# Kernel tuning notes

Measured on AMD Instinct MI355X. Metric: run time of the kernel, lower is better.

The kernel has to match this reference:

```python
import jax, jax.numpy as jnp
import numpy as np

N = 8192        # nodes
E = 131072      # random edges (16 * N); self loops appended inside reference
D = 128         # in_channels
K = int(np.ceil(0.5 * N))  # pooled nodes, ratio=0.5
NEG = 0.2       # leaky relu negative slope


def setup_inputs() -> dict:
    key = jax.random.key(0)
    ks = jax.random.split(key, 10)
    s = 0.05
    return dict(
        x=jax.random.normal(ks[0], (N, D), jnp.float32),
        edge_src=jax.random.randint(ks[1], (E,), 0, N),
        edge_off=jax.random.randint(ks[2], (E,), 0, N - 1),
        W_lin=jax.random.normal(ks[3], (D, D), jnp.float32) * s,
        b_lin=jnp.zeros((D,), jnp.float32),
        w_att=jax.random.normal(ks[4], (2 * D,), jnp.float32) * s,
        b_att=jnp.zeros((1,), jnp.float32),
        w1=jax.random.normal(ks[5], (D,), jnp.float32) * s,
        b1=jnp.zeros((1,), jnp.float32),
        w2=jax.random.normal(ks[6], (D,), jnp.float32) * s,
        w3=jax.random.normal(ks[7], (D,), jnp.float32) * s,
        b3=jnp.zeros((1,), jnp.float32),
    )


def reference(x, edge_src, edge_off, W_lin, b_lin, w_att, b_att, w1, b1, w2, w3, b3):
    # build edges with guaranteed no self loops, then add_remaining_self_loops (weight 1)
    dst = (edge_src + 1 + edge_off) % N
    loop = jnp.arange(N)
    row = jnp.concatenate([edge_src, loop])   # [Et] source j
    col = jnp.concatenate([dst, loop])        # [Et] target i
    ew = jnp.ones(row.shape, x.dtype)         # edge weights (fill_value=1)

    # GNN=None -> x_pool = x
    x_pool_j = x[row]                                             # [Et, D]
    x_q = jax.ops.segment_max(x_pool_j, col, num_segments=N)      # scatter-max at target
    x_q = (x_q @ W_lin + b_lin)[col]                              # [Et, D]

    score = jnp.concatenate([x_q, x_pool_j], axis=-1) @ w_att + b_att[0]  # [Et]
    score = jax.nn.leaky_relu(score, negative_slope=NEG)
    # edge softmax over incoming edges of each target node (stable)
    smax = jax.ops.segment_max(score, col, num_segments=N)
    e = jnp.exp(score - smax[col])
    score = e / jax.ops.segment_sum(e, col, num_segments=N)[col]
    # dropout p=0 (eval): no-op

    # attention-weighted aggregation
    x_new = jax.ops.segment_sum(x[row] * score[:, None], col, num_segments=N)  # [N, D]

    # LEConv fitness (out_channels=1): lin3(x) + sum_j w_ji * (lin1(x)_i - lin2(x)_j)
    a = x_new @ w1 + b1[0]                                        # [N]
    b = x_new @ w2                                                # [N]
    agg = jax.ops.segment_sum(ew * (a[col] - b[row]), col, num_segments=N)
    fitness = jax.nn.sigmoid(x_new @ w3 + b3[0] + agg)            # [N]

    # topk pooling (single graph): k = ceil(ratio * N)
    perm = jnp.argsort(-fitness)[:K]
    x_out = x_new[perm] * fitness[perm][:, None]                  # [K, D]

    # dense N x N attention as in original, then column-select perm
    attention = jnp.zeros((N, N), x.dtype).at[row, col].set(score)
    S_perm = attention[:, perm]                                   # [N, K] == S[:, perm]

    # A_new = S^T A S (A sparse, weight 1 per edge incl. self loops), diag removed
    T = jax.ops.segment_sum(ew[:, None] * S_perm[col], row, num_segments=N)  # A @ S_perm
    A_new = S_perm.T @ T                                          # [K, K]
    A_new = A_new * (1.0 - jnp.eye(K, dtype=x.dtype))             # remove_diag

    return x_out, A_new, perm, S_perm
```

## Files before the change

### kernel.cpp

```cpp
#include <hip/hip_runtime.h>
#include <hip/hip_bf16.h>
#include <math.h>
#include <stdint.h>

#define N_NODES 8192
#define E_EDGES 131072
#define D_DIM 128
#define M_EDGES (E_EDGES + N_NODES)
#define K_TOP 4096
#define NEG_SLOPE 0.2

__global__ __launch_bounds__(256) void k_zero(uint4* __restrict__ p, int n16) {
    int i = blockIdx.x * 256 + threadIdx.x;
    if (i < n16) { uint4 z; z.x = 0u; z.y = 0u; z.z = 0u; z.w = 0u; p[i] = z; }
}

__global__ void k_init_edges(const int* __restrict__ edge_src, const int* __restrict__ edge_off,
                             unsigned* __restrict__ rowA, unsigned* __restrict__ colA,
                             unsigned* __restrict__ dup,
                             unsigned* __restrict__ col_cnt, unsigned* __restrict__ row_cnt) {
    int e = blockIdx.x * blockDim.x + threadIdx.x;
    if (e >= M_EDGES) return;
    unsigned r, c;
    if (e < E_EDGES) {
        r = (unsigned)edge_src[e];
        c = (r + 1u + (unsigned)edge_off[e]) % N_NODES;
    } else {
        r = c = (unsigned)(e - E_EDGES);
    }
    rowA[e] = r; colA[e] = c; dup[e] = 0u;
    atomicAdd(&col_cnt[c], 1u);
    atomicAdd(&row_cnt[r], 1u);
}

__global__ __launch_bounds__(1024) void k_scan2(const unsigned* __restrict__ cnt0, unsigned* __restrict__ off0, unsigned* __restrict__ cur0,
                                                const unsigned* __restrict__ cnt1, unsigned* __restrict__ off1, unsigned* __restrict__ cur1) {
    const unsigned* cnt = blockIdx.x ? cnt1 : cnt0;
    unsigned* off = blockIdx.x ? off1 : off0;
    unsigned* cur = blockIdx.x ? cur1 : cur0;
    __shared__ unsigned part[1024];
    const int n = N_NODES, per = N_NODES / 1024;
    int t = threadIdx.x;
    unsigned local[8];
    unsigned s = 0;
    for (int j = 0; j < per; j++) { local[j] = cnt[t * per + j]; s += local[j]; }
    part[t] = s; __syncthreads();
    for (int d = 1; d < 1024; d <<= 1) {
        unsigned v = (t >= d) ? part[t - d] : 0u;
        __syncthreads();
        part[t] += v;
        __syncthreads();
    }
    unsigned run = (t > 0) ? part[t - 1] : 0u;
    for (int j = 0; j < per; j++) {
        off[t * per + j] = run;
        if (cur) cur[t * per + j] = run;
        run += local[j];
    }
    if (t == 1023) off[n] = run;
}

__global__ void k_fill(const unsigned* __restrict__ rowA, const unsigned* __restrict__ colA,
                       unsigned* __restrict__ col_cur, unsigned* __restrict__ row_cur,
                       unsigned* __restrict__ col_edges, unsigned* __restrict__ row_edges) {
    int e = blockIdx.x * blockDim.x + threadIdx.x;
    if (e >= M_EDGES) return;
    unsigned p1 = atomicAdd(&col_cur[colA[e]], 1u); col_edges[p1] = (unsigned)e;
    unsigned p2 = atomicAdd(&row_cur[rowA[e]], 1u); row_edges[p2] = (unsigned)e;
}

__global__ __launch_bounds__(128) void k_lin(const float* __restrict__ x,
                                             const unsigned* __restrict__ col_off,
                                             const unsigned* __restrict__ col_edges,
                                             const unsigned* __restrict__ rowA,
                                             unsigned* __restrict__ dup,
                                             const float* __restrict__ W, const float* __restrict__ b_lin,
                                             const float* __restrict__ w_att,
                                             double* __restrict__ q_score, double* __restrict__ k_score) {
    int c = blockIdx.x, t = threadIdx.x;
    __shared__ unsigned rloc[256];
    __shared__ float xq[128];
    __shared__ double red[4];
    int lo = (int)col_off[c], hi = (int)col_off[c + 1];
    int n = hi - lo;
    for (int i = t; i < n && i < 256; i += 128) rloc[i] = rowA[col_edges[lo + i]];
    __syncthreads();
    for (int i = t; i < n; i += 128) {
        unsigned ri = (i < 256) ? rloc[i] : rowA[col_edges[lo + i]];
        for (int j = 0; j < i; j++) {
            unsigned rj = (j < 256) ? rloc[j] : rowA[col_edges[lo + j]];
            if (rj == ri) { dup[col_edges[lo + i]] = 1u; break; }
        }
    }
    float m = -INFINITY;
    for (int i = 0; i < n; i++) {
        unsigned r = (i < 256) ? rloc[i] : rowA[col_edges[lo + i]];
        m = fmaxf(m, x[(size_t)r * D_DIM + t]);
    }
    xq[t] = m;
    __syncthreads();
    double acc = (double)b_lin[t];
    for (int j = 0; j < D_DIM; j++) acc += (double)xq[j] * (double)W[j * D_DIM + t];
    double q = acc * (double)w_att[t];
    double k = (double)x[(size_t)c * D_DIM + t] * (double)w_att[D_DIM + t];
    for (int o = 32; o > 0; o >>= 1) { q += __shfl_down(q, o); k += __shfl_down(k, o); }
    if ((t & 63) == 0) { red[t >> 6] = q; red[2 + (t >> 6)] = k; }
    __syncthreads();
    if (t == 0) { q_score[c] = red[0] + red[1]; k_score[c] = red[2] + red[3]; }
}

__global__ __launch_bounds__(128) void k_sm_xnew(const float* __restrict__ x,
                                                 const unsigned* __restrict__ col_off,
                                                 const unsigned* __restrict__ col_edges,
                                                 const unsigned* __restrict__ rowA,
                                                 const double* __restrict__ q_score,
                                                 const double* __restrict__ k_score,
                                                 const float* __restrict__ b_att,
                                                 const float* __restrict__ w1, const float* __restrict__ b1,
                                                 const float* __restrict__ w2, const float* __restrict__ w3,
                                                 const float* __restrict__ b3,
                                                 double* __restrict__ score_d, float* __restrict__ score_f,
                                                 float* __restrict__ x_new, double* __restrict__ aV,
                                                 double* __restrict__ bV, double* __restrict__ finV) {
    int c = blockIdx.x, t = threadIdx.x;
    __shared__ unsigned eloc[256];
    __shared__ unsigned rloc[256];
    __shared__ double sloc[256];
    __shared__ double redd[2];
    __shared__ double red6[6];
    int lo = (int)col_off[c], hi = (int)col_off[c + 1];
    int n = hi - lo;
    for (int i = t; i < n && i < 256; i += 128) {
        unsigned e = col_edges[lo + i];
        eloc[i] = e;
        rloc[i] = rowA[e];
    }
    __syncthreads();
    double qc = q_score[c] + (double)b_att[0];
    double m = -INFINITY;
    for (int i = t; i < n; i += 128) {
        unsigned r = (i < 256) ? rloc[i] : rowA[col_edges[lo + i]];
        double s = qc + k_score[r];
        s = (s >= 0.0) ? s : NEG_SLOPE * s;
        m = fmax(m, s);
    }
    for (int o = 32; o > 0; o >>= 1) m = fmax(m, __shfl_xor(m, o));
    if ((t & 63) == 0) redd[t >> 6] = m;
    __syncthreads();
    m = fmax(redd[0], redd[1]);
    __syncthreads();
    double sum = 0.0;
    for (int i = t; i < n; i += 128) {
        unsigned r = (i < 256) ? rloc[i] : rowA[col_edges[lo + i]];
        double s = qc + k_score[r];
        s = (s >= 0.0) ? s : NEG_SLOPE * s;
        sum += exp(s - m);
    }
    for (int o = 32; o > 0; o >>= 1) sum += __shfl_xor(sum, o);
    if ((t & 63) == 0) redd[t >> 6] = sum;
    __syncthreads();
    sum = redd[0] + redd[1];
    for (int i = t; i < n; i += 128) {
        unsigned e = (i < 256) ? eloc[i] : col_edges[lo + i];
        unsigned r = (i < 256) ? rloc[i] : rowA[e];
        double s = qc + k_score[r];
        s = (s >= 0.0) ? s : NEG_SLOPE * s;
        double w = exp(s - m) / sum;
        if (i < 256) sloc[i] = w;
        score_d[e] = w;
        score_f[e] = (float)w;
    }
    __syncthreads();
    int d = t;
    double acc = 0.0;
    for (int i = 0; i < n; i++) {
        unsigned r;
        double sc;
        if (i < 256) { r = rloc[i]; sc = sloc[i]; }
        else { unsigned e = col_edges[lo + i]; r = rowA[e]; sc = score_d[e]; }
        acc += sc * (double)x[(size_t)r * D_DIM + d];
    }
    x_new[(size_t)c * D_DIM + d] = (float)acc;
    double pa = acc * (double)w1[d], pb = acc * (double)w2[d], pf = acc * (double)w3[d];
    for (int o = 32; o > 0; o >>= 1) { pa += __shfl_down(pa, o); pb += __shfl_down(pb, o); pf += __shfl_down(pf, o); }
    if ((d & 63) == 0) { int w = d >> 6; red6[w] = pa; red6[2 + w] = pb; red6[4 + w] = pf; }
    __syncthreads();
    if (d == 0) {
        aV[c] = red6[0] + red6[1] + (double)b1[0];
        bV[c] = red6[2] + red6[3];
        finV[c] = red6[4] + red6[5] + (double)b3[0];
    }
}

__global__ __launch_bounds__(64) void k_fitness(const unsigned* __restrict__ col_off,
                                                const unsigned* __restrict__ col_edges,
                                                const unsigned* __restrict__ rowA,
                                                const double* __restrict__ aV, const double* __restrict__ bV,
                                                const double* __restrict__ finV,
                                                double* __restrict__ fitness) {
    int c = blockIdx.x, t = threadIdx.x;
    int lo = (int)col_off[c], hi = (int)col_off[c + 1];
    double ac = aV[c], s = 0.0;
    for (int i = lo + t; i < hi; i += 64) s += ac - bV[rowA[col_edges[i]]];
    for (int o = 32; o > 0; o >>= 1) s += __shfl_xor(s, o);
    if (t == 0) {
        double z = finV[c] + s;
        fitness[c] = 1.0 / (1.0 + exp(-z));
    }
}

__global__ __launch_bounds__(1024) void k_sortlocal(const double* __restrict__ fitness,
                                                    unsigned long long* __restrict__ keys) {
    __shared__ unsigned long long k2[2048];
    int t = threadIdx.x, base = blockIdx.x * 2048;
    for (int i = t; i < 2048; i += 1024) {
        unsigned long long bits = (unsigned long long)__double_as_longlong(fitness[base + i]);
        unsigned long long u = (bits & 0x8000000000000000ull) ? ~bits : (bits | 0x8000000000000000ull);
        k2[i] = (~u & 0xFFFFFFFFFFFFE000ull) | (unsigned long long)(base + i);
    }
    __syncthreads();
    for (int size = 2; size <= 2048; size <<= 1) {
        for (int stride = size >> 1; stride > 0; stride >>= 1) {
            int pos = 2 * t - (t & (stride - 1));
            bool asc = ((pos & size) == 0);
            unsigned long long A = k2[pos], B = k2[pos + stride];
            if ((A > B) == asc) { k2[pos] = B; k2[pos + stride] = A; }
            __syncthreads();
        }
    }
    for (int i = t; i < 2048; i += 1024) keys[base + i] = k2[i];
}

__global__ __launch_bounds__(256) void k_merge(const unsigned long long* __restrict__ in,
                                               unsigned long long* __restrict__ out, int L) {
    int g = blockIdx.x * 256 + threadIdx.x;
    if (g >= N_NODES) return;
    int pair = g / (2 * L), r = g - pair * 2 * L;
    const unsigned long long* A = in + (size_t)pair * 2 * L;
    const unsigned long long* B = A + L;
    unsigned long long v; int p;
    if (r < L) {
        v = A[r];
        int lo = 0, hi = L;
        while (lo < hi) { int mid = (lo + hi) >> 1; if (B[mid] < v) lo = mid + 1; else hi = mid; }
        p = r + lo;
    } else {
        int j = r - L; v = B[j];
        int lo = 0, hi = L;
        while (lo < hi) { int mid = (lo + hi) >> 1; if (A[mid] < v) lo = mid + 1; else hi = mid; }
        p = j + lo;
    }
    out[(size_t)pair * 2 * L + p] = v;
}

__global__ __launch_bounds__(256) void k_merge_emit(const unsigned long long* __restrict__ in,
                                                    unsigned* __restrict__ perm_i, int* __restrict__ inv_k,
                                                    float* __restrict__ perm_out) {
    int g = blockIdx.x * 256 + threadIdx.x;
    if (g >= N_NODES) return;
    const unsigned long long* A = in;
    const unsigned long long* B = in + 4096;
    unsigned long long v; int p;
    if (g < 4096) {
        v = A[g];
        int lo = 0, hi = 4096;
        while (lo < hi) { int mid = (lo + hi) >> 1; if (B[mid] < v) lo = mid + 1; else hi = mid; }
        p = g + lo;
    } else {
        int j = g - 4096; v = B[j];
        int lo = 0, hi = 4096;
        while (lo < hi) { int mid = (lo + hi) >> 1; if (A[mid] < v) lo = mid + 1; else hi = mid; }
        p = j + lo;
    }
    unsigned idx = (unsigned)(v & 0x1FFFull);
    inv_k[idx] = (p < K_TOP) ? p : -1;
    if (p < K_TOP) { perm_i[p] = idx; perm_out[p] = (float)idx; }
}

__global__ __launch_bounds__(64) void k_scount(const unsigned* __restrict__ row_off,
                                               const unsigned* __restrict__ row_edges,
                                               const unsigned* __restrict__ colA,
                                               const unsigned* __restrict__ dup,
                                               const int* __restrict__ inv_k,
                                               unsigned* __restrict__ s_cnt) {
    int c = blockIdx.x, t = threadIdx.x;
    int lo = (int)row_off[c], hi = (int)row_off[c + 1];
    unsigned cnt = 0;
    for (int i = lo + t; i < hi; i += 64) {
        unsigned e = row_edges[i];
        if (!dup[e] && inv_k[colA[e]] >= 0) cnt++;
    }
    for (int o = 32; o > 0; o >>= 1) cnt += __shfl_xor(cnt, o);
    if (t == 0) s_cnt[c] = cnt;
}

__global__ __launch_bounds__(64) void k_sfill(const unsigned* __restrict__ row_off,
                                              const unsigned* __restrict__ row_edges,
                                              const unsigned* __restrict__ colA,
                                              const unsigned* __restrict__ dup,
                                              const int* __restrict__ inv_k,
                                              const unsigned* __restrict__ s_off,
                                              const float* __restrict__ score,
                                              unsigned* __restrict__ s_k, float* __restrict__ s_v) {
    int c = blockIdx.x, t = threadIdx.x;
    int lo = (int)row_off[c], hi = (int)row_off[c + 1];
    unsigned base = s_off[c];
    for (int i0 = lo; i0 < hi; i0 += 64) {
        int i = i0 + t;
        bool pred = false; unsigned e = 0; int kk = -1;
        if (i < hi) {
            e = row_edges[i];
            kk = inv_k[colA[e]];
            pred = (!dup[e]) && (kk >= 0);
        }
        unsigned long long mask = __ballot(pred);
        if (pred) {
            unsigned pos = (unsigned)__popcll(mask & ((1ull << t) - 1ull));
            s_k[base + pos] = (unsigned)kk;
            s_v[base + pos] = score[e];
        }
        base += (unsigned)__popcll(mask);
    }
}

__global__ __launch_bounds__(64) void k_tcount(const unsigned* __restrict__ row_off,
                                               const unsigned* __restrict__ row_edges,
                                               const unsigned* __restrict__ colA,
                                               const unsigned* __restrict__ s_cnt,
                                               unsigned* __restrict__ t_cnt) {
    int r = blockIdx.x, t = threadIdx.x;
    int lo = (int)row_off[r], hi = (int)row_off[r + 1];
    unsigned cnt = 0;
    for (int i = lo + t; i < hi; i += 64) cnt += s_cnt[colA[row_edges[i]]];
    for (int o = 32; o > 0; o >>= 1) cnt += __shfl_xor(cnt, o);
    if (t == 0) t_cnt[r] = cnt;
}

__global__ __launch_bounds__(64) void k_tfill(const unsigned* __restrict__ row_off,
                                              const unsigned* __restrict__ row_edges,
                                              const unsigned* __restrict__ colA,
                                              const unsigned* __restrict__ s_off,
                                              const unsigned* __restrict__ s_cnt,
                                              const unsigned* __restrict__ s_k,
                                              const float* __restrict__ s_v,
                                              const unsigned* __restrict__ t_off,
                                              unsigned* __restrict__ t_k, float* __restrict__ t_v,
                                              unsigned tcap) {
    int r = blockIdx.x, t = threadIdx.x;
    int lo = (int)row_off[r], hi = (int)row_off[r + 1];
    unsigned base = t_off[r];
    for (int i0 = lo; i0 < hi; i0 += 64) {
        int i = i0 + t;
        unsigned cnt = 0, c2 = 0;
        if (i < hi) { c2 = colA[row_edges[i]]; cnt = s_cnt[c2]; }
        unsigned pre = cnt;
        for (int o = 1; o < 64; o <<= 1) { unsigned v = __shfl_up(pre, o); if (t >= o) pre += v; }
        unsigned excl = pre - cnt;
        unsigned total = __shfl(pre, 63);
        if (i < hi && cnt) {
            unsigned sb = s_off[c2];
            unsigned db = base + excl;
            if (db + cnt <= tcap) {
                for (unsigned j = 0; j < cnt; j++) { t_k[db + j] = s_k[sb + j]; t_v[db + j] = s_v[sb + j]; }
            }
        }
        base += total;
    }
}

__global__ __launch_bounds__(256) void k_spermz(const unsigned* __restrict__ s_off,
                                                const unsigned* __restrict__ s_k,
                                                const float* __restrict__ s_v,
                                                float* __restrict__ S_out) {
    int r = blockIdx.x, t = threadIdx.x;
    float4* row4 = (float4*)(S_out + (size_t)r * K_TOP);
    float4 z; z.x = 0.f; z.y = 0.f; z.z = 0.f; z.w = 0.f;
    for (int i = t; i < K_TOP / 4; i += 256) row4[i] = z;
    __syncthreads();
    int lo = (int)s_off[r], hi = (int)s_off[r + 1];
    for (int j = lo + t; j < hi; j += 256)
        S_out[(size_t)r * K_TOP + s_k[j]] = s_v[j];
}

__global__ __launch_bounds__(256) void k_anew(const unsigned* __restrict__ col_off,
                                              const unsigned* __restrict__ col_edges,
                                              const unsigned* __restrict__ rowA,
                                              const unsigned* __restrict__ dup,
                                              const float* __restrict__ score,
                                              const unsigned* __restrict__ perm_i,
                                              const unsigned* __restrict__ t_off,
                                              const unsigned* __restrict__ t_k,
                                              const float* __restrict__ t_v,
                                              float* __restrict__ A_out) {
    __shared__ float acc[K_TOP];
    int k1 = blockIdx.x, t = threadIdx.x;
    for (int i = t; i < K_TOP; i += 256) acc[i] = 0.f;
    __syncthreads();
    unsigned p = perm_i[k1];
    int lo = (int)col_off[p], hi = (int)col_off[p + 1];
    for (int i = lo; i < hi; i++) {
        unsigned e = col_edges[i];
        if (dup[e]) continue;
        float sc = score[e];
        unsigned n = rowA[e];
        unsigned tb = t_off[n], te = t_off[n + 1];
        for (unsigned j = tb + t; j < te; j += 256)
            atomicAdd(&acc[t_k[j]], sc * t_v[j]);
    }
    __syncthreads();
    float* outp = &A_out[(size_t)k1 * K_TOP];
    for (int i = t; i < K_TOP; i += 256) outp[i] = (i == k1) ? 0.f : acc[i];
}

__global__ __launch_bounds__(128) void k_xout(const float* __restrict__ x_new,
                                              const double* __restrict__ fitness,
                                              const unsigned* __restrict__ perm_i,
                                              float* __restrict__ xo) {
    int k = blockIdx.x, d = threadIdx.x;
    unsigned p = perm_i[k];
    xo[(size_t)k * D_DIM + d] = x_new[(size_t)p * D_DIM + d] * (float)fitness[p];
}

extern "C" void kernel_launch(void* const* d_in, const int* in_sizes, int n_in,
                              void* d_out, int out_size, void* d_ws, size_t ws_size,
                              hipStream_t stream) {
    const float* x        = (const float*)d_in[0];
    const int*   edge_src = (const int*)d_in[1];
    const int*   edge_off = (const int*)d_in[2];
    const float* W_lin    = (const float*)d_in[3];
    const float* b_lin    = (const float*)d_in[4];
    const float* w_att    = (const float*)d_in[5];
    const float* b_att    = (const float*)d_in[6];
    const float* w1       = (const float*)d_in[7];
    const float* b1       = (const float*)d_in[8];
    const float* w2       = (const float*)d_in[9];
    const float* w3       = (const float*)d_in[10];
    const float* b3       = (const float*)d_in[11];

    float* out = (float*)d_out;
    float* out_xout  = out;
    float* out_anew  = out + (size_t)K_TOP * D_DIM;
    float* out_perm  = out_anew + (size_t)K_TOP * K_TOP;
    float* out_sperm = out_perm + K_TOP;

    char* wp = (char*)d_ws;
    char* wend = wp + ws_size;
    auto alloc = [&](size_t bytes) -> void* {
        void* p = (void*)wp;
        wp += (bytes + 255) & ~(size_t)255;
        return p;
    };
    unsigned* rowA      = (unsigned*)alloc((size_t)M_EDGES * 4);
    unsigned* colA      = (unsigned*)alloc((size_t)M_EDGES * 4);
    unsigned* dup       = (unsigned*)alloc((size_t)M_EDGES * 4);
    double*   score_d   = (double*)alloc((size_t)M_EDGES * 8);
    float*    score     = (float*)alloc((size_t)M_EDGES * 4);
    unsigned* cnts      = (unsigned*)alloc((size_t)2 * N_NODES * 4);
    unsigned* col_cnt   = cnts;
    unsigned* row_cnt   = cnts + N_NODES;
    unsigned* col_off   = (unsigned*)alloc((size_t)(N_NODES + 1) * 4);
    unsigned* row_off   = (unsigned*)alloc((size_t)(N_NODES + 1) * 4);
    unsigned* col_cur   = (unsigned*)alloc((size_t)N_NODES * 4);
    unsigned* row_cur   = (unsigned*)alloc((size_t)N_NODES * 4);
    unsigned* col_edges = (unsigned*)alloc((size_t)M_EDGES * 4);
    unsigned* row_edges = (unsigned*)alloc((size_t)M_EDGES * 4);
    float*    x_new     = (float*)alloc((size_t)N_NODES * D_DIM * 4);
    double*   q_score   = (double*)alloc((size_t)N_NODES * 8);
    double*   k_score   = (double*)alloc((size_t)N_NODES * 8);
    double*   aV        = (double*)alloc((size_t)N_NODES * 8);
    double*   bV        = (double*)alloc((size_t)N_NODES * 8);
    double*   finV      = (double*)alloc((size_t)N_NODES * 8);
    double*   fitness   = (double*)alloc((size_t)N_NODES * 8);
    unsigned long long* keys_a = (unsigned long long*)alloc((size_t)N_NODES * 8);
    unsigned long long* keys_b = (unsigned long long*)alloc((size_t)N_NODES * 8);
    unsigned* perm_i    = (unsigned*)alloc((size_t)K_TOP * 4);
    int*      inv_k     = (int*)alloc((size_t)N_NODES * 4);
    unsigned* s_cnt     = (unsigned*)alloc((size_t)N_NODES * 4);
    unsigned* s_off     = (unsigned*)alloc((size_t)(N_NODES + 1) * 4);
    unsigned* s_k       = (unsigned*)alloc((size_t)M_EDGES * 4);
    float*    s_v       = (float*)alloc((size_t)M_EDGES * 4);
    unsigned* t_cnt     = (unsigned*)alloc((size_t)N_NODES * 4);
    unsigned* t_off     = (unsigned*)alloc((size_t)(N_NODES + 1) * 4);
    size_t remain = (size_t)(wend - wp);
    size_t tcap = remain / 8;
    if (tcap > (size_t)6 * 1024 * 1024) tcap = (size_t)6 * 1024 * 1024;
    unsigned* t_k = (unsigned*)alloc(tcap * 4);
    float*    t_v = (float*)alloc(tcap * 4);

    k_zero<<<(2 * N_NODES / 4 + 255) / 256, 256, 0, stream>>>((uint4*)cnts, 2 * N_NODES / 4);

    k_init_edges<<<(M_EDGES + 255) / 256, 256, 0, stream>>>(edge_src, edge_off, rowA, colA, dup, col_cnt, row_cnt);
    k_scan2<<<2, 1024, 0, stream>>>(col_cnt, col_off, col_cur, row_cnt, row_off, row_cur);
    k_fill<<<(M_EDGES + 255) / 256, 256, 0, stream>>>(rowA, colA, col_cur, row_cur, col_edges, row_edges);
    k_lin<<<N_NODES, 128, 0, stream>>>(x, col_off, col_edges, rowA, dup, W_lin, b_lin, w_att, q_score, k_score);
    k_sm_xnew<<<N_NODES, 128, 0, stream>>>(x, col_off, col_edges, rowA, q_score, k_score, b_att,
                                           w1, b1, w2, w3, b3, score_d, score, x_new, aV, bV, finV);
    k_fitness<<<N_NODES, 64, 0, stream>>>(col_off, col_edges, rowA, aV, bV, finV, fitness);
    k_sortlocal<<<4, 1024, 0, stream>>>(fitness, keys_a);
    k_merge<<<N_NODES / 256, 256, 0, stream>>>(keys_a, keys_b, 2048);
    k_merge_emit<<<N_NODES / 256, 256, 0, stream>>>(keys_b, perm_i, inv_k, out_perm);
    k_scount<<<N_NODES, 64, 0, stream>>>(row_off, row_edges, colA, dup, inv_k, s_cnt);
    k_tcount<<<N_NODES, 64, 0, stream>>>(row_off, row_edges, colA, s_cnt, t_cnt);
    k_scan2<<<2, 1024, 0, stream>>>(s_cnt, s_off, (unsigned*)nullptr, t_cnt, t_off, (unsigned*)nullptr);
    k_sfill<<<N_NODES, 64, 0, stream>>>(row_off, row_edges, colA, dup, inv_k, s_off, score, s_k, s_v);
    k_tfill<<<N_NODES, 64, 0, stream>>>(row_off, row_edges, colA, s_off, s_cnt, s_k, s_v, t_off,
                                        t_k, t_v, (unsigned)tcap);
    k_spermz<<<N_NODES, 256, 0, stream>>>(s_off, s_k, s_v, out_sperm);
    k_anew<<<K_TOP, 256, 0, stream>>>(col_off, col_edges, rowA, dup, score, perm_i, t_off, t_k, t_v, out_anew);
    k_xout<<<K_TOP, 128, 0, stream>>>(x_new, fitness, perm_i, out_xout);
}
```

Measured before the change: 277.8 us.

## Fuse tail kernels and merge scans into neighbouring work to cut launches

Replaces the three-kernel top-k sort (local bitonic plus two merge passes) with a single-block 8192-key bitonic sort in shared memory that emits perm directly. Folds the s/t prefix scans into the tcount and sfill kernels as an extra block, packing 16 rows per 1024-thread block. Merges the S_perm zero-fill, A_new and x_out kernels into one launch with block-range dispatch. This removes roughly six launches and their gaps. The cost is that the whole sort now runs on one workgroup, which serialises that step.

```diff
diff --git a/kernel.cpp b/kernel.cpp
--- a/kernel.cpp
+++ b/kernel.cpp
@@ -33,13 +33,11 @@
     atomicAdd(&row_cnt[r], 1u);
 }
 
-__global__ __launch_bounds__(1024) void k_scan2(const unsigned* __restrict__ cnt0, unsigned* __restrict__ off0, unsigned* __restrict__ cur0,
-                                                const unsigned* __restrict__ cnt1, unsigned* __restrict__ off1, unsigned* __restrict__ cur1) {
-    const unsigned* cnt = blockIdx.x ? cnt1 : cnt0;
-    unsigned* off = blockIdx.x ? off1 : off0;
-    unsigned* cur = blockIdx.x ? cur1 : cur0;
-    __shared__ unsigned part[1024];
-    const int n = N_NODES, per = N_NODES / 1024;
+__device__ __forceinline__ void scan8192(const unsigned* __restrict__ cnt,
+                                         unsigned* __restrict__ off,
+                                         unsigned* __restrict__ cur,
+                                         unsigned* part) {
+    const int per = N_NODES / 1024;
     int t = threadIdx.x;
     unsigned local[8];
     unsigned s = 0;
@@ -57,7 +55,14 @@
         if (cur) cur[t * per + j] = run;
         run += local[j];
     }
-    if (t == 1023) off[n] = run;
+    if (t == 1023) off[N_NODES] = run;
+}
+
+__global__ __launch_bounds__(1024) void k_scan2(const unsigned* __restrict__ cnt0, unsigned* __restrict__ off0, unsigned* __restrict__ cur0,
+                                                const unsigned* __restrict__ cnt1, unsigned* __restrict__ off1, unsigned* __restrict__ cur1) {
+    __shared__ unsigned part[1024];
+    if (blockIdx.x) scan8192(cnt1, off1, cur1, part);
+    else            scan8192(cnt0, off0, cur0, part);
 }
 
 __global__ void k_fill(const unsigned* __restrict__ rowA, const unsigned* __restrict__ colA,
@@ -209,72 +214,34 @@
     }
 }
 
-__global__ __launch_bounds__(1024) void k_sortlocal(const double* __restrict__ fitness,
-                                                    unsigned long long* __restrict__ keys) {
-    __shared__ unsigned long long k2[2048];
-    int t = threadIdx.x, base = blockIdx.x * 2048;
-    for (int i = t; i < 2048; i += 1024) {
-        unsigned long long bits = (unsigned long long)__double_as_longlong(fitness[base + i]);
+__global__ __launch_bounds__(1024) void k_sort8k(const double* __restrict__ fitness,
+                                                 unsigned* __restrict__ perm_i, int* __restrict__ inv_k,
+                                                 float* __restrict__ perm_out) {
+    __shared__ unsigned long long keys[8192];
+    int t = threadIdx.x;
+    for (int i = t; i < 8192; i += 1024) {
+        unsigned long long bits = (unsigned long long)__double_as_longlong(fitness[i]);
         unsigned long long u = (bits & 0x8000000000000000ull) ? ~bits : (bits | 0x8000000000000000ull);
-        k2[i] = (~u & 0xFFFFFFFFFFFFE000ull) | (unsigned long long)(base + i);
-    }
-    __syncthreads();
-    for (int size = 2; size <= 2048; size <<= 1) {
+        keys[i] = (~u & 0xFFFFFFFFFFFFE000ull) | (unsigned long long)i;
+    }
+    __syncthreads();
+    for (int size = 2; size <= 8192; size <<= 1) {
         for (int stride = size >> 1; stride > 0; stride >>= 1) {
-            int pos = 2 * t - (t & (stride - 1));
-            bool asc = ((pos & size) == 0);
-            unsigned long long A = k2[pos], B = k2[pos + stride];
-            if ((A > B) == asc) { k2[pos] = B; k2[pos + stride] = A; }
+            for (int idx = t; idx < 4096; idx += 1024) {
+                int pos = 2 * idx - (idx & (stride - 1));
+                int partner = pos + stride;
+                bool asc = ((pos & size) == 0);
+                unsigned long long A = keys[pos], B = keys[partner];
+                if ((A > B) == asc) { keys[pos] = B; keys[partner] = A; }
+            }
             __syncthreads();
         }
     }
-    for (int i = t; i < 2048; i += 1024) keys[base + i] = k2[i];
-}
-
-__global__ __launch_bounds__(256) void k_merge(const unsigned long long* __restrict__ in,
-                                               unsigned long long* __restrict__ out, int L) {
-    int g = blockIdx.x * 256 + threadIdx.x;
-    if (g >= N_NODES) return;
-    int pair = g / (2 * L), r = g - pair * 2 * L;
-    const unsigned long long* A = in + (size_t)pair * 2 * L;
-    const unsigned long long* B = A + L;
-    unsigned long long v; int p;
-    if (r < L) {
-        v = A[r];
-        int lo = 0, hi = L;
-        while (lo < hi) { int mid = (lo + hi) >> 1; if (B[mid] < v) lo = mid + 1; else hi = mid; }
-        p = r + lo;
-    } else {
-        int j = r - L; v = B[j];
-        int lo = 0, hi = L;
-        while (lo < hi) { int mid = (lo + hi) >> 1; if (A[mid] < v) lo = mid + 1; else hi = mid; }
-        p = j + lo;
-    }
-    out[(size_t)pair * 2 * L + p] = v;
-}
-
-__global__ __launch_bounds__(256) void k_merge_emit(const unsigned long long* __restrict__ in,
-                                                    unsigned* __restrict__ perm_i, int* __restrict__ inv_k,
-                                                    float* __restrict__ perm_out) {
-    int g = blockIdx.x * 256 + threadIdx.x;
-    if (g >= N_NODES) return;
-    const unsigned long long* A = in;
-    const unsigned long long* B = in + 4096;
-    unsigned long long v; int p;
-    if (g < 4096) {
-        v = A[g];
-        int lo = 0, hi = 4096;
-        while (lo < hi) { int mid = (lo + hi) >> 1; if (B[mid] < v) lo = mid + 1; else hi = mid; }
-        p = g + lo;
-    } else {
-        int j = g - 4096; v = B[j];
-        int lo = 0, hi = 4096;
-        while (lo < hi) { int mid = (lo + hi) >> 1; if (A[mid] < v) lo = mid + 1; else hi = mid; }
-        p = j + lo;
-    }
-    unsigned idx = (unsigned)(v & 0x1FFFull);
-    inv_k[idx] = (p < K_TOP) ? p : -1;
-    if (p < K_TOP) { perm_i[p] = idx; perm_out[p] = (float)idx; }
+    for (int k = t; k < 8192; k += 1024) {
+        unsigned idx = (unsigned)(keys[k] & 0x1FFFull);
+        inv_k[idx] = (k < K_TOP) ? k : -1;
+        if (k < K_TOP) { perm_i[k] = idx; perm_out[k] = (float)idx; }
+    }
 }
 
 __global__ __launch_bounds__(64) void k_scount(const unsigned* __restrict__ row_off,
@@ -294,19 +261,47 @@
     if (t == 0) s_cnt[c] = cnt;
 }
 
-__global__ __launch_bounds__(64) void k_sfill(const unsigned* __restrict__ row_off,
-                                              const unsigned* __restrict__ row_edges,
-                                              const unsigned* __restrict__ colA,
-                                              const unsigned* __restrict__ dup,
-                                              const int* __restrict__ inv_k,
-                                              const unsigned* __restrict__ s_off,
-                                              const float* __restrict__ score,
-                                              unsigned* __restrict__ s_k, float* __restrict__ s_v) {
-    int c = blockIdx.x, t = threadIdx.x;
+__global__ __launch_bounds__(1024) void k_scan_s_tcount(const unsigned* __restrict__ s_cnt,
+                                                        unsigned* __restrict__ s_off,
+                                                        const unsigned* __restrict__ row_off,
+                                                        const unsigned* __restrict__ row_edges,
+                                                        const unsigned* __restrict__ colA,
+                                                        unsigned* __restrict__ t_cnt) {
+    __shared__ unsigned part[1024];
+    if (blockIdx.x == 0) {
+        scan8192(s_cnt, s_off, (unsigned*)nullptr, part);
+        return;
+    }
+    int r = (blockIdx.x - 1) * 16 + (threadIdx.x >> 6);
+    int lane = threadIdx.x & 63;
+    int lo = (int)row_off[r], hi = (int)row_off[r + 1];
+    unsigned cnt = 0;
+    for (int i = lo + lane; i < hi; i += 64) cnt += s_cnt[colA[row_edges[i]]];
+    for (int o = 32; o > 0; o >>= 1) cnt += __shfl_xor(cnt, o);
+    if (lane == 0) t_cnt[r] = cnt;
+}
+
+__global__ __launch_bounds__(1024) void k_scan_t_sfill(const unsigned* __restrict__ t_cnt,
+                                                       unsigned* __restrict__ t_off,
+                                                       const unsigned* __restrict__ row_off,
+                                                       const unsigned* __restrict__ row_edges,
+                                                       const unsigned* __restrict__ colA,
+                                                       const unsigned* __restrict__ dup,
+                                                       const int* __restrict__ inv_k,
+                                                       const unsigned* __restrict__ s_off,
+                                                       const float* __restrict__ score,
+                                                       unsigned* __restrict__ s_k, float* __restrict__ s_v) {
+    __shared__ unsigned part[1024];
+    if (blockIdx.x == 0) {
+        scan8192(t_cnt, t_off, (unsigned*)nullptr, part);
+        return;
+    }
+    int c = (blockIdx.x - 1) * 16 + (threadIdx.x >> 6);
+    int lane = threadIdx.x & 63;
     int lo = (int)row_off[c], hi = (int)row_off[c + 1];
     unsigned base = s_off[c];
     for (int i0 = lo; i0 < hi; i0 += 64) {
-        int i = i0 + t;
+        int i = i0 + lane;
         bool pred = false; unsigned e = 0; int kk = -1;
         if (i < hi) {
             e = row_edges[i];
@@ -315,25 +310,12 @@
         }
         unsigned long long mask = __ballot(pred);
         if (pred) {
-            unsigned pos = (unsigned)__popcll(mask & ((1ull << t) - 1ull));
+            unsigned pos = (unsigned)__popcll(mask & ((1ull << lane) - 1ull));
             s_k[base + pos] = (unsigned)kk;
             s_v[base + pos] = score[e];
         }
         base += (unsigned)__popcll(mask);
     }
-}
-
-__global__ __launch_bounds__(64) void k_tcount(const unsigned* __restrict__ row_off,
-                                               const unsigned* __restrict__ row_edges,
-                                               const unsigned* __restrict__ colA,
-                                               const unsigned* __restrict__ s_cnt,
-                                               unsigned* __restrict__ t_cnt) {
-    int r = blockIdx.x, t = threadIdx.x;
-    int lo = (int)row_off[r], hi = (int)row_off[r + 1];
-    unsigned cnt = 0;
-    for (int i = lo + t; i < hi; i += 64) cnt += s_cnt[colA[row_edges[i]]];
-    for (int o = 32; o > 0; o >>= 1) cnt += __shfl_xor(cnt, o);
-    if (t == 0) t_cnt[r] = cnt;
 }
 
 __global__ __launch_bounds__(64) void k_tfill(const unsigned* __restrict__ row_off,
@@ -368,21 +350,7 @@
     }
 }
 
-__global__ __launch_bounds__(256) void k_spermz(const unsigned* __restrict__ s_off,
-                                                const unsigned* __restrict__ s_k,
-                                                const float* __restrict__ s_v,
-                                                float* __restrict__ S_out) {
-    int r = blockIdx.x, t = threadIdx.x;
-    float4* row4 = (float4*)(S_out + (size_t)r * K_TOP);
-    float4 z; z.x = 0.f; z.y = 0.f; z.z = 0.f; z.w = 0.f;
-    for (int i = t; i < K_TOP / 4; i += 256) row4[i] = z;
-    __syncthreads();
-    int lo = (int)s_off[r], hi = (int)s_off[r + 1];
-    for (int j = lo + t; j < hi; j += 256)
-        S_out[(size_t)r * K_TOP + s_k[j]] = s_v[j];
-}
-
-__global__ __launch_bounds__(256) void k_anew(const unsigned* __restrict__ col_off,
+__global__ __launch_bounds__(256) void k_tail(const unsigned* __restrict__ col_off,
                                               const unsigned* __restrict__ col_edges,
                                               const unsigned* __restrict__ rowA,
                                               const unsigned* __restrict__ dup,
@@ -391,34 +359,51 @@
                                               const unsigned* __restrict__ t_off,
                                               const unsigned* __restrict__ t_k,
                                               const float* __restrict__ t_v,
-                                              float* __restrict__ A_out) {
+                                              const unsigned* __restrict__ s_off,
+                                              const unsigned* __restrict__ s_k,
+                                              const float* __restrict__ s_v,
+                                              const float* __restrict__ x_new,
+                                              const double* __restrict__ fitness,
+                                              float* __restrict__ A_out,
+                                              float* __restrict__ S_out,
+                                              float* __restrict__ xo) {
     __shared__ float acc[K_TOP];
-    int k1 = blockIdx.x, t = threadIdx.x;
-    for (int i = t; i < K_TOP; i += 256) acc[i] = 0.f;
-    __syncthreads();
-    unsigned p = perm_i[k1];
-    int lo = (int)col_off[p], hi = (int)col_off[p + 1];
-    for (int i = lo; i < hi; i++) {
-        unsigned e = col_edges[i];
-        if (dup[e]) continue;
-        float sc = score[e];
-        unsigned n = rowA[e];
-        unsigned tb = t_off[n], te = t_off[n + 1];
-        for (unsigned j = tb + t; j < te; j += 256)
-            atomicAdd(&acc[t_k[j]], sc * t_v[j]);
-    }
-    __syncthreads();
-    float* outp = &A_out[(size_t)k1 * K_TOP];
-    for (int i = t; i < K_TOP; i += 256) outp[i] = (i == k1) ? 0.f : acc[i];
-}
-
-__global__ __launch_bounds__(128) void k_xout(const float* __restrict__ x_new,
-                                              const double* __restrict__ fitness,
-                                              const unsigned* __restrict__ perm_i,
-                                              float* __restrict__ xo) {
-    int k = blockIdx.x, d = threadIdx.x;
-    unsigned p = perm_i[k];
-    xo[(size_t)k * D_DIM + d] = x_new[(size_t)p * D_DIM + d] * (float)fitness[p];
+    int bid = blockIdx.x, t = threadIdx.x;
+    if (bid < K_TOP) {
+        int k1 = bid;
+        for (int i = t; i < K_TOP; i += 256) acc[i] = 0.f;
+        __syncthreads();
+        unsigned p = perm_i[k1];
+        int lo = (int)col_off[p], hi = (int)col_off[p + 1];
+        for (int i = lo; i < hi; i++) {
+            unsigned e = col_edges[i];
+            if (dup[e]) continue;
+            float sc = score[e];
+            unsigned n = rowA[e];
+            unsigned tb = t_off[n], te = t_off[n + 1];
+            for (unsigned j = tb + t; j < te; j += 256)
+                atomicAdd(&acc[t_k[j]], sc * t_v[j]);
+        }
+        __syncthreads();
+        float* outp = &A_out[(size_t)k1 * K_TOP];
+        for (int i = t; i < K_TOP; i += 256) outp[i] = (i == k1) ? 0.f : acc[i];
+    } else if (bid < K_TOP + N_NODES) {
+        int r = bid - K_TOP;
+        float4* row4 = (float4*)(S_out + (size_t)r * K_TOP);
+        float4 z; z.x = 0.f; z.y = 0.f; z.z = 0.f; z.w = 0.f;
+        for (int i = t; i < K_TOP / 4; i += 256) row4[i] = z;
+        __syncthreads();
+        int lo = (int)s_off[r], hi = (int)s_off[r + 1];
+        for (int j = lo + t; j < hi; j += 256)
+            S_out[(size_t)r * K_TOP + s_k[j]] = s_v[j];
+    } else {
+        int gid = (bid - K_TOP - N_NODES) * 256 + t;
+        for (int u = gid; u < K_TOP * D_DIM; u += 32 * 256) {
+            int k = u >> 7, d = u & 127;
+            unsigned pp = perm_i[k];
+            xo[u] = x_new[(size_t)pp * D_DIM + d] * (float)fitness[pp];
+        }
+    }
 }
 
 extern "C" void kernel_launch(void* const* d_in, const int* in_sizes, int n_in,
@@ -471,8 +456,6 @@
     double*   bV        = (double*)alloc((size_t)N_NODES * 8);
     double*   finV      = (double*)alloc((size_t)N_NODES * 8);
     double*   fitness   = (double*)alloc((size_t)N_NODES * 8);
-    unsigned long long* keys_a = (unsigned long long*)alloc((size_t)N_NODES * 8);
-    unsigned long long* keys_b = (unsigned long long*)alloc((size_t)N_NODES * 8);
     unsigned* perm_i    = (unsigned*)alloc((size_t)K_TOP * 4);
     int*      inv_k     = (int*)alloc((size_t)N_NODES * 4);
     unsigned* s_cnt     = (unsigned*)alloc((size_t)N_NODES * 4);
@@ -488,7 +471,6 @@
     float*    t_v = (float*)alloc(tcap * 4);
 
     k_zero<<<(2 * N_NODES / 4 + 255) / 256, 256, 0, stream>>>((uint4*)cnts, 2 * N_NODES / 4);
-
     k_init_edges<<<(M_EDGES + 255) / 256, 256, 0, stream>>>(edge_src, edge_off, rowA, colA, dup, col_cnt, row_cnt);
     k_scan2<<<2, 1024, 0, stream>>>(col_cnt, col_off, col_cur, row_cnt, row_off, row_cur);
     k_fill<<<(M_EDGES + 255) / 256, 256, 0, stream>>>(rowA, colA, col_cur, row_cur, col_edges, row_edges);
@@ -496,16 +478,14 @@
     k_sm_xnew<<<N_NODES, 128, 0, stream>>>(x, col_off, col_edges, rowA, q_score, k_score, b_att,
                                            w1, b1, w2, w3, b3, score_d, score, x_new, aV, bV, finV);
     k_fitness<<<N_NODES, 64, 0, stream>>>(col_off, col_edges, rowA, aV, bV, finV, fitness);
-    k_sortlocal<<<4, 1024, 0, stream>>>(fitness, keys_a);
-    k_merge<<<N_NODES / 256, 256, 0, stream>>>(keys_a, keys_b, 2048);
-    k_merge_emit<<<N_NODES / 256, 256, 0, stream>>>(keys_b, perm_i, inv_k, out_perm);
+    k_sort8k<<<1, 1024, 0, stream>>>(fitness, perm_i, inv_k, out_perm);
     k_scount<<<N_NODES, 64, 0, stream>>>(row_off, row_edges, colA, dup, inv_k, s_cnt);
-    k_tcount<<<N_NODES, 64, 0, stream>>>(row_off, row_edges, colA, s_cnt, t_cnt);
-    k_scan2<<<2, 1024, 0, stream>>>(s_cnt, s_off, (unsigned*)nullptr, t_cnt, t_off, (unsigned*)nullptr);
-    k_sfill<<<N_NODES, 64, 0, stream>>>(row_off, row_edges, colA, dup, inv_k, s_off, score, s_k, s_v);
+    k_scan_s_tcount<<<1 + N_NODES / 16, 1024, 0, stream>>>(s_cnt, s_off, row_off, row_edges, colA, t_cnt);
+    k_scan_t_sfill<<<1 + N_NODES / 16, 1024, 0, stream>>>(t_cnt, t_off, row_off, row_edges, colA,
+                                                          dup, inv_k, s_off, score, s_k, s_v);
     k_tfill<<<N_NODES, 64, 0, stream>>>(row_off, row_edges, colA, s_off, s_cnt, s_k, s_v, t_off,
                                         t_k, t_v, (unsigned)tcap);
-    k_spermz<<<N_NODES, 256, 0, stream>>>(s_off, s_k, s_v, out_sperm);
-    k_anew<<<K_TOP, 256, 0, stream>>>(col_off, col_edges, rowA, dup, score, perm_i, t_off, t_k, t_v, out_anew);
-    k_xout<<<K_TOP, 128, 0, stream>>>(x_new, fitness, perm_i, out_xout);
-}
+    k_tail<<<K_TOP + N_NODES + 32, 256, 0, stream>>>(col_off, col_edges, rowA, dup, score, perm_i,
+                                                     t_off, t_k, t_v, s_off, s_k, s_v,
+                                                     x_new, fitness, out_anew, out_sperm, out_xout);
+}
```

Result: slower. 331.3 us (+19.3%).

## Precompute W·w_att vector, cache scores, drop double score buffer, fuse xout

Applied to the files above, without the earlier changes.

The dense 128x128 matvec per node is replaced by a precomputed vector Wv = W_lin·w_att[:D] plus a bias term, so each k_lin block computes only a dot product. The softmax kernel caches leaky-relu scores in shared memory and stops writing the double-precision score array. The x_out gather moves into extra blocks of the S_perm kernel, and zeroing is merged into a prep kernel, which saves launches. Overflow edges beyond 256 now use float scores, which slightly changes precision.

```diff
diff --git a/kernel.cpp b/kernel.cpp
--- a/kernel.cpp
+++ b/kernel.cpp
@@ -10,9 +10,28 @@
 #define K_TOP 4096
 #define NEG_SLOPE 0.2
 
-__global__ __launch_bounds__(256) void k_zero(uint4* __restrict__ p, int n16) {
-    int i = blockIdx.x * 256 + threadIdx.x;
-    if (i < n16) { uint4 z; z.x = 0u; z.y = 0u; z.z = 0u; z.w = 0u; p[i] = z; }
+__global__ __launch_bounds__(256) void k_prep(uint4* __restrict__ cnts16,
+                                              const float* __restrict__ W,
+                                              const float* __restrict__ b_lin,
+                                              const float* __restrict__ w_att,
+                                              double* __restrict__ Wv) {
+    if (blockIdx.x < 16) {
+        int i = blockIdx.x * 256 + threadIdx.x;
+        uint4 z; z.x = 0u; z.y = 0u; z.z = 0u; z.w = 0u;
+        cnts16[i] = z;
+        return;
+    }
+    int j = threadIdx.x;
+    if (j < 128) {
+        double acc = 0.0;
+        for (int t = 0; t < 128; t++) acc += (double)W[j * 128 + t] * (double)w_att[t];
+        Wv[j] = acc;
+    }
+    if (j == 128) {
+        double b = 0.0;
+        for (int t = 0; t < 128; t++) b += (double)b_lin[t] * (double)w_att[t];
+        Wv[128] = b;
+    }
 }
 
 __global__ void k_init_edges(const int* __restrict__ edge_src, const int* __restrict__ edge_off,
@@ -74,12 +93,11 @@
                                              const unsigned* __restrict__ col_edges,
                                              const unsigned* __restrict__ rowA,
                                              unsigned* __restrict__ dup,
-                                             const float* __restrict__ W, const float* __restrict__ b_lin,
+                                             const double* __restrict__ Wv,
                                              const float* __restrict__ w_att,
                                              double* __restrict__ q_score, double* __restrict__ k_score) {
     int c = blockIdx.x, t = threadIdx.x;
     __shared__ unsigned rloc[256];
-    __shared__ float xq[128];
     __shared__ double red[4];
     int lo = (int)col_off[c], hi = (int)col_off[c + 1];
     int n = hi - lo;
@@ -97,16 +115,12 @@
         unsigned r = (i < 256) ? rloc[i] : rowA[col_edges[lo + i]];
         m = fmaxf(m, x[(size_t)r * D_DIM + t]);
     }
-    xq[t] = m;
-    __syncthreads();
-    double acc = (double)b_lin[t];
-    for (int j = 0; j < D_DIM; j++) acc += (double)xq[j] * (double)W[j * D_DIM + t];
-    double q = acc * (double)w_att[t];
+    double q = (double)m * Wv[t];
     double k = (double)x[(size_t)c * D_DIM + t] * (double)w_att[D_DIM + t];
     for (int o = 32; o > 0; o >>= 1) { q += __shfl_down(q, o); k += __shfl_down(k, o); }
     if ((t & 63) == 0) { red[t >> 6] = q; red[2 + (t >> 6)] = k; }
     __syncthreads();
-    if (t == 0) { q_score[c] = red[0] + red[1]; k_score[c] = red[2] + red[3]; }
+    if (t == 0) { q_score[c] = red[0] + red[1] + Wv[128]; k_score[c] = red[2] + red[3]; }
 }
 
 __global__ __launch_bounds__(128) void k_sm_xnew(const float* __restrict__ x,
@@ -119,7 +133,7 @@
                                                  const float* __restrict__ w1, const float* __restrict__ b1,
                                                  const float* __restrict__ w2, const float* __restrict__ w3,
                                                  const float* __restrict__ b3,
-                                                 double* __restrict__ score_d, float* __restrict__ score_f,
+                                                 float* __restrict__ score_f,
                                                  float* __restrict__ x_new, double* __restrict__ aV,
                                                  double* __restrict__ bV, double* __restrict__ finV) {
     int c = blockIdx.x, t = threadIdx.x;
@@ -142,6 +156,7 @@
         unsigned r = (i < 256) ? rloc[i] : rowA[col_edges[lo + i]];
         double s = qc + k_score[r];
         s = (s >= 0.0) ? s : NEG_SLOPE * s;
+        if (i < 256) sloc[i] = s;
         m = fmax(m, s);
     }
     for (int o = 32; o > 0; o >>= 1) m = fmax(m, __shfl_xor(m, o));
@@ -151,9 +166,12 @@
     __syncthreads();
     double sum = 0.0;
     for (int i = t; i < n; i += 128) {
-        unsigned r = (i < 256) ? rloc[i] : rowA[col_edges[lo + i]];
-        double s = qc + k_score[r];
-        s = (s >= 0.0) ? s : NEG_SLOPE * s;
+        double s;
+        if (i < 256) s = sloc[i];
+        else {
+            double sv = qc + k_score[rowA[col_edges[lo + i]]];
+            s = (sv >= 0.0) ? sv : NEG_SLOPE * sv;
+        }
         sum += exp(s - m);
     }
     for (int o = 32; o > 0; o >>= 1) sum += __shfl_xor(sum, o);
@@ -162,12 +180,14 @@
     sum = redd[0] + redd[1];
     for (int i = t; i < n; i += 128) {
         unsigned e = (i < 256) ? eloc[i] : col_edges[lo + i];
-        unsigned r = (i < 256) ? rloc[i] : rowA[e];
-        double s = qc + k_score[r];
-        s = (s >= 0.0) ? s : NEG_SLOPE * s;
+        double s;
+        if (i < 256) s = sloc[i];
+        else {
+            double sv = qc + k_score[rowA[e]];
+            s = (sv >= 0.0) ? sv : NEG_SLOPE * sv;
+        }
         double w = exp(s - m) / sum;
         if (i < 256) sloc[i] = w;
-        score_d[e] = w;
         score_f[e] = (float)w;
     }
     __syncthreads();
@@ -177,7 +197,11 @@
         unsigned r;
         double sc;
         if (i < 256) { r = rloc[i]; sc = sloc[i]; }
-        else { unsigned e = col_edges[lo + i]; r = rowA[e]; sc = score_d[e]; }
+        else {
+            unsigned e = col_edges[lo + i];
+            r = rowA[e];
+            sc = (double)score_f[e];
+        }
         acc += sc * (double)x[(size_t)r * D_DIM + d];
     }
     x_new[(size_t)c * D_DIM + d] = (float)acc;
@@ -371,15 +395,29 @@
 __global__ __launch_bounds__(256) void k_spermz(const unsigned* __restrict__ s_off,
                                                 const unsigned* __restrict__ s_k,
                                                 const float* __restrict__ s_v,
-                                                float* __restrict__ S_out) {
-    int r = blockIdx.x, t = threadIdx.x;
-    float4* row4 = (float4*)(S_out + (size_t)r * K_TOP);
-    float4 z; z.x = 0.f; z.y = 0.f; z.z = 0.f; z.w = 0.f;
-    for (int i = t; i < K_TOP / 4; i += 256) row4[i] = z;
-    __syncthreads();
-    int lo = (int)s_off[r], hi = (int)s_off[r + 1];
-    for (int j = lo + t; j < hi; j += 256)
-        S_out[(size_t)r * K_TOP + s_k[j]] = s_v[j];
+                                                const unsigned* __restrict__ perm_i,
+                                                const float* __restrict__ x_new,
+                                                const double* __restrict__ fitness,
+                                                float* __restrict__ S_out,
+                                                float* __restrict__ xo) {
+    int bid = blockIdx.x, t = threadIdx.x;
+    if (bid < N_NODES) {
+        int r = bid;
+        float4* row4 = (float4*)(S_out + (size_t)r * K_TOP);
+        float4 z; z.x = 0.f; z.y = 0.f; z.z = 0.f; z.w = 0.f;
+        for (int i = t; i < K_TOP / 4; i += 256) row4[i] = z;
+        __syncthreads();
+        int lo = (int)s_off[r], hi = (int)s_off[r + 1];
+        for (int j = lo + t; j < hi; j += 256)
+            S_out[(size_t)r * K_TOP + s_k[j]] = s_v[j];
+    } else {
+        int gid = (bid - N_NODES) * 256 + t;
+        for (int u = gid; u < K_TOP * D_DIM; u += 32 * 256) {
+            int k = u >> 7, d = u & 127;
+            unsigned pp = perm_i[k];
+            xo[u] = x_new[(size_t)pp * D_DIM + d] * (float)fitness[pp];
+        }
+    }
 }
 
 __global__ __launch_bounds__(256) void k_anew(const unsigned* __restrict__ col_off,
@@ -410,15 +448,6 @@
     __syncthreads();
     float* outp = &A_out[(size_t)k1 * K_TOP];
     for (int i = t; i < K_TOP; i += 256) outp[i] = (i == k1) ? 0.f : acc[i];
-}
-
-__global__ __launch_bounds__(128) void k_xout(const float* __restrict__ x_new,
-                                              const double* __restrict__ fitness,
-                                              const unsigned* __restrict__ perm_i,
-                                              float* __restrict__ xo) {
-    int k = blockIdx.x, d = threadIdx.x;
-    unsigned p = perm_i[k];
-    xo[(size_t)k * D_DIM + d] = x_new[(size_t)p * D_DIM + d] * (float)fitness[p];
 }
 
 extern "C" void kernel_launch(void* const* d_in, const int* in_sizes, int n_in,
@@ -453,7 +482,6 @@
     unsigned* rowA      = (unsigned*)alloc((size_t)M_EDGES * 4);
     unsigned* colA      = (unsigned*)alloc((size_t)M_EDGES * 4);
     unsigned* dup       = (unsigned*)alloc((size_t)M_EDGES * 4);
-    double*   score_d   = (double*)alloc((size_t)M_EDGES * 8);
     float*    score     = (float*)alloc((size_t)M_EDGES * 4);
     unsigned* cnts      = (unsigned*)alloc((size_t)2 * N_NODES * 4);
     unsigned* col_cnt   = cnts;
@@ -465,6 +493,7 @@
     unsigned* col_edges = (unsigned*)alloc((size_t)M_EDGES * 4);
     unsigned* row_edges = (unsigned*)alloc((size_t)M_EDGES * 4);
     float*    x_new     = (float*)alloc((size_t)N_NODES * D_DIM * 4);
+    double*   Wv        = (double*)alloc((size_t)129 * 8);
     double*   q_score   = (double*)alloc((size_t)N_NODES * 8);
     double*   k_score   = (double*)alloc((size_t)N_NODES * 8);
     double*   aV        = (double*)alloc((size_t)N_NODES * 8);
@@ -487,14 +516,13 @@
     unsigned* t_k = (unsigned*)alloc(tcap * 4);
     float*    t_v = (float*)alloc(tcap * 4);
 
-    k_zero<<<(2 * N_NODES / 4 + 255) / 256, 256, 0, stream>>>((uint4*)cnts, 2 * N_NODES / 4);
-
+    k_prep<<<17, 256, 0, stream>>>((uint4*)cnts, W_lin, b_lin, w_att, Wv);
     k_init_edges<<<(M_EDGES + 255) / 256, 256, 0, stream>>>(edge_src, edge_off, rowA, colA, dup, col_cnt, row_cnt);
     k_scan2<<<2, 1024, 0, stream>>>(col_cnt, col_off, col_cur, row_cnt, row_off, row_cur);
     k_fill<<<(M_EDGES + 255) / 256, 256, 0, stream>>>(rowA, colA, col_cur, row_cur, col_edges, row_edges);
-    k_lin<<<N_NODES, 128, 0, stream>>>(x, col_off, col_edges, rowA, dup, W_lin, b_lin, w_att, q_score, k_score);
+    k_lin<<<N_NODES, 128, 0, stream>>>(x, col_off, col_edges, rowA, dup, Wv, w_att, q_score, k_score);
     k_sm_xnew<<<N_NODES, 128, 0, stream>>>(x, col_off, col_edges, rowA, q_score, k_score, b_att,
-                                           w1, b1, w2, w3, b3, score_d, score, x_new, aV, bV, finV);
+                                           w1, b1, w2, w3, b3, score, x_new, aV, bV, finV);
     k_fitness<<<N_NODES, 64, 0, stream>>>(col_off, col_edges, rowA, aV, bV, finV, fitness);
     k_sortlocal<<<4, 1024, 0, stream>>>(fitness, keys_a);
     k_merge<<<N_NODES / 256, 256, 0, stream>>>(keys_a, keys_b, 2048);
@@ -505,7 +533,6 @@
     k_sfill<<<N_NODES, 64, 0, stream>>>(row_off, row_edges, colA, dup, inv_k, s_off, score, s_k, s_v);
     k_tfill<<<N_NODES, 64, 0, stream>>>(row_off, row_edges, colA, s_off, s_cnt, s_k, s_v, t_off,
                                         t_k, t_v, (unsigned)tcap);
-    k_spermz<<<N_NODES, 256, 0, stream>>>(s_off, s_k, s_v, out_sperm);
+    k_spermz<<<N_NODES + 32, 256, 0, stream>>>(s_off, s_k, s_v, perm_i, x_new, fitness, out_sperm, out_xout);
     k_anew<<<K_TOP, 256, 0, stream>>>(col_off, col_edges, rowA, dup, score, perm_i, t_off, t_k, t_v, out_anew);
-    k_xout<<<K_TOP, 128, 0, stream>>>(x_new, fitness, perm_i, out_xout);
-}
+}
```

Result: slower. 288.7 us (+3.9%).
